# Optimization experiments

Measured on AMD Instinct MI355X. Metric: run time of the kernel, lower is better.

The kernel has to match this reference:

```python
import jax, jax.numpy as jnp
import numpy as np

N_NODES = 100000
N_EDGES = 1600000
F_IN, F1, F2, F3 = 128, 128, 128, 64


def setup_inputs() -> dict:
    key = jax.random.key(0)
    ks = jax.random.split(key, 10)
    edge_index = jax.random.randint(ks[0], (2, N_EDGES), 0, N_NODES, dtype=jnp.int64)
    x = jax.random.normal(ks[1], (N_NODES, F_IN), dtype=jnp.float32)
    def glorot(k, fi, fo):
        s = (6.0 / (fi + fo)) ** 0.5
        return jax.random.uniform(k, (fi, fo), jnp.float32, -s, s)
    return {
        "edge_index": edge_index,
        "x": x,
        "W1": glorot(ks[2], F_IN, F1), "b1": jnp.zeros((F1,), jnp.float32),
        "W2": glorot(ks[3], F1, F2), "b2": jnp.zeros((F2,), jnp.float32),
        "W3": glorot(ks[4], F2, F3), "b3": jnp.zeros((F3,), jnp.float32),
        "W_att": glorot(ks[5], F3, F3),
    }


def _gcn_conv(x, W, b, src, dst, deg_inv_sqrt):
    h = x @ W  # [N, Fo]
    norm = deg_inv_sqrt[src] * deg_inv_sqrt[dst]  # [E]
    agg = jax.ops.segment_sum(h[src] * norm[:, None], dst, num_segments=x.shape[0])
    agg = agg + h * (deg_inv_sqrt * deg_inv_sqrt)[:, None]  # self-loop term
    return agg + b


def _attention_pool(emb, W_att):
    # SimGNN attention pooling
    ctx = jnp.tanh(jnp.mean(emb @ W_att, axis=0))          # [F3]
    scores = jax.nn.sigmoid(emb @ ctx)                      # [N]
    return emb.T @ scores[:, None]                          # [F3, 1]


def reference(edge_index, x, W1, b1, W2, b2, W3, b3, W_att):
    src, dst = edge_index[0], edge_index[1]
    n = x.shape[0]
    deg = jax.ops.segment_sum(jnp.ones_like(src, dtype=x.dtype), dst, num_segments=n) + 1.0
    dis = jax.lax.rsqrt(deg)
    h = jax.nn.relu(_gcn_conv(x, W1, b1, src, dst, dis))
    h = jax.nn.relu(_gcn_conv(h, W2, b2, src, dst, dis))
    h = _gcn_conv(h, W3, b3, src, dst, dis)                 # abstract_features [N, F3]
    pooled = _attention_pool(h, W_att)                      # [F3, 1]
    return h, pooled
```

## Files before the change

kernel.cpp:

```cpp
#include <hip/hip_runtime.h>
#include <hip/hip_bf16.h>

#define NN 100000
#define NE 1600000
#define NR 100032
#define NB2 196
#define NBLK 391
#define EPB 4096

#if defined(__has_builtin)
#  if __has_builtin(__builtin_amdgcn_cvt_pk_f32_fp8) && \
      __has_builtin(__builtin_amdgcn_cvt_pk_fp8_f32) && \
      __has_builtin(__builtin_amdgcn_cvt_f32_fp8)
#    define HWF8 1
#  endif
#endif

typedef float f32x2 __attribute__((ext_vector_type(2)));
typedef float f32x4 __attribute__((ext_vector_type(4)));
typedef short bf16x8 __attribute__((ext_vector_type(8)));

static __device__ __forceinline__ float bf2f(__hip_bfloat16 v) { return __bfloat162float(v); }
static __device__ __forceinline__ float bfu(unsigned short w) {
    return __uint_as_float((unsigned)w << 16);
}

static __device__ __forceinline__ float f8d_sw(unsigned b) {
    unsigned e = (b >> 3) & 15u, m = b & 7u;
    float mag;
    if (e == 0) mag = (float)m * 0.001953125f;
    else        mag = __uint_as_float(((e + 120u) << 23) | (m << 20));
    return (b & 0x80u) ? -mag : mag;
}
static __device__ __forceinline__ unsigned char f8e_sw(float x) {
    unsigned u = __float_as_uint(x);
    unsigned s = (u >> 31) << 7;
    unsigned au = u & 0x7fffffffu;
    if (au >= 0x43E00000u) return (unsigned char)(s | 0x7Eu);
    if (au <  0x3A800000u) return (unsigned char)s;
    if (au <  0x3C800000u) {
        float a = __uint_as_float(au);
        int m = (int)rintf(a * 512.0f);
        if (m >= 8) return (unsigned char)(s | 0x08u);
        return (unsigned char)(s | (unsigned)m);
    }
    au += 0x80000u;
    if (au >= 0x43E00000u) return (unsigned char)(s | 0x7Eu);
    unsigned e = (au >> 23) - 120u;
    unsigned m = (au >> 20) & 7u;
    return (unsigned char)(s | (e << 3) | m);
}

static __device__ __forceinline__ float f8d1(unsigned b) {
#ifdef HWF8
    return __builtin_amdgcn_cvt_f32_fp8((int)b, 0);
#else
    return f8d_sw(b);
#endif
}
static __device__ __forceinline__ void f8d2(unsigned short v, float& x0, float& x1) {
#ifdef HWF8
    f32x2 r = __builtin_amdgcn_cvt_pk_f32_fp8((int)(unsigned)v, false);
    x0 = r.x; x1 = r.y;
#else
    x0 = f8d_sw(v & 255u); x1 = f8d_sw(v >> 8);
#endif
}
static __device__ __forceinline__ void f8d4(unsigned u, float* o) {
#ifdef HWF8
    f32x2 lo = __builtin_amdgcn_cvt_pk_f32_fp8((int)u, false);
    f32x2 hi = __builtin_amdgcn_cvt_pk_f32_fp8((int)u, true);
    o[0] = lo.x; o[1] = lo.y; o[2] = hi.x; o[3] = hi.y;
#else
    o[0] = f8d_sw(u & 255u); o[1] = f8d_sw((u >> 8) & 255u);
    o[2] = f8d_sw((u >> 16) & 255u); o[3] = f8d_sw(u >> 24);
#endif
}
static __device__ __forceinline__ unsigned short f8e2(float a, float b) {
#ifdef HWF8
    float ca = fminf(fmaxf(a, -448.0f), 448.0f);
    float cb = fminf(fmaxf(b, -448.0f), 448.0f);
    int p = __builtin_amdgcn_cvt_pk_fp8_f32(ca, cb, 0, false);
    return (unsigned short)(p & 0xFFFF);
#else
    return (unsigned short)f8e_sw(a) | ((unsigned short)f8e_sw(b) << 8);
#endif
}
static __device__ __forceinline__ unsigned char f8e1(float a) {
    return (unsigned char)(f8e2(a, 0.0f) & 0xFF);
}
static __device__ __forceinline__ unsigned bfpack(float lo, float hi) {
    return (__float_as_uint(lo) >> 16) | (__float_as_uint(hi) & 0xFFFF0000u);
}

static __device__ __forceinline__ void fma8(float* acc, uint2 v, float w) {
    float o[8];
    f8d4(v.x, o); f8d4(v.y, o + 4);
#pragma unroll
    for (int k = 0; k < 8; k++) acc[k] = fmaf(o[k], w, acc[k]);
}

__global__ void k_probe1(const unsigned short* __restrict__ xw,
                         const int* __restrict__ ei, int* __restrict__ raw) {
    int i = blockIdx.x * 256 + threadIdx.x;
    int nan = ((xw[i] & 0x7F80u) == 0x7F80u) ? 1 : 0;
    int odd = (ei[2 * i + 1] != 0) ? 1 : 0;
    unsigned long long bn = __ballot(nan);
    unsigned long long bo = __ballot(odd);
    if ((threadIdx.x & 63) == 0) {
        if (bn) atomicAdd(&raw[0], __popcll(bn));
        if (bo) atomicAdd(&raw[1], __popcll(bo));
    }
}
__global__ void k_probe2(const int* __restrict__ raw, int* __restrict__ flags) {
    if (threadIdx.x == 0) {
        flags[0] = (raw[0] > 0) ? 1 : 0;
        flags[1] = (raw[1] == 0) ? 1 : 0;
    }
}

static __device__ __forceinline__ int e_src(const int* ei, int e, int f64) {
    int v = f64 ? ei[2 * e] : ei[e];
    return min(max(v, 0), NN - 1);
}
static __device__ __forceinline__ int e_dst(const int* ei, int e, int f64) {
    int v = f64 ? ei[2 * (NE + e)] : ei[NE + e];
    return min(max(v, 0), NN - 1);
}
static __device__ __forceinline__ float ldx(const void* p, long long i, int f32) {
    return f32 ? ((const float*)p)[i] : bf2f(((const __hip_bfloat16*)p)[i]);
}

__global__ void cvt_params(const void* W1, const void* b1, const void* W2, const void* b2,
                           const void* W3, const void* b3, const void* Wa,
                           unsigned short* W1b, unsigned short* W2b, unsigned short* W3b,
                           float* b1f, float* b2f, float* b3f, float* Waf,
                           const int* flags) {
    int i = blockIdx.x * blockDim.x + threadIdx.x;
    int f = flags[0];
    if (i < 16384) {
        int j = i & 7, l = (i >> 3) & 63, c = (i >> 9) & 7, kc = i >> 12;
        int k = kc * 32 + ((l >> 4)) * 8 + j;
        int col = c * 16 + (l & 15);
        W1b[i] = __bfloat16_as_ushort(__float2bfloat16(ldx(W1, k * 128 + col, f)));
        W2b[i] = __bfloat16_as_ushort(__float2bfloat16(ldx(W2, k * 128 + col, f)));
    }
    if (i < 8192) {
        int j = i & 7, l = (i >> 3) & 63, c = (i >> 9) & 3, kc = i >> 11;
        int k = kc * 32 + ((l >> 4)) * 8 + j;
        int col = c * 16 + (l & 15);
        W3b[i] = __bfloat16_as_ushort(__float2bfloat16(ldx(W3, k * 64 + col, f)));
    }
    if (i < 4096)  Waf[i] = ldx(Wa, i, f);
    if (i < 128)   { b1f[i] = ldx(b1, i, f); b2f[i] = ldx(b2, i, f); }
    if (i < 64)    b3f[i] = ldx(b3, i, f);
}

__global__ void k_cvtx(const void* __restrict__ x, unsigned char* __restrict__ P,
                       const int* __restrict__ flags) {
    int i = blockIdx.x * blockDim.x + threadIdx.x;
    if (i >= (NN * 128) / 4) return;
    unsigned pk;
    if (flags[0]) {
        float4 v = ((const float4*)x)[i];
        pk = (unsigned)f8e2(v.x, v.y) | ((unsigned)f8e2(v.z, v.w) << 16);
    } else {
        ushort4 v = ((const ushort4*)x)[i];
        pk = (unsigned)f8e2(bfu(v.x), bfu(v.y)) | ((unsigned)f8e2(bfu(v.z), bfu(v.w)) << 16);
    }
    ((unsigned*)P)[i] = pk;
}

__global__ __launch_bounds__(256) void k_hist(const int* __restrict__ ei,
                                              int* __restrict__ ghist,
                                              const int* __restrict__ flags) {
    __shared__ int h[NB2];
    int blk = blockIdx.x, t = threadIdx.x;
    for (int i = t; i < NB2; i += 256) h[i] = 0;
    __syncthreads();
    int f64 = flags[1];
    int e0 = blk * EPB;
    for (int i = t; i < EPB; i += 256) {
        int e = e0 + i;
        if (e < NE) atomicAdd(&h[e_dst(ei, e, f64) >> 9], 1);
    }
    __syncthreads();
    for (int i = t; i < NB2; i += 256) ghist[blk * NB2 + i] = h[i];
}

__global__ __launch_bounds__(256) void k_off(const int* __restrict__ ghist,
                                             int* __restrict__ cbase,
                                             int* __restrict__ offm,
                                             int* __restrict__ rowptr) {
    __shared__ int tot[NB2];
    int t = threadIdx.x;
    if (t < NB2) {
        int s = 0;
        for (int blk = 0; blk < NBLK; blk++) s += ghist[blk * NB2 + t];
        tot[t] = s;
    }
    __syncthreads();
    if (t == 0) {
        int run = 0;
        for (int b = 0; b < NB2; b++) { cbase[b] = run; run += tot[b]; }
        cbase[NB2] = run;
        rowptr[NN] = run;
    }
    __syncthreads();
    if (t < NB2) {
        int run = cbase[t];
        for (int blk = 0; blk < NBLK; blk++) {
            offm[blk * NB2 + t] = run;
            run += ghist[blk * NB2 + t];
        }
    }
}

__global__ __launch_bounds__(256) void k_scatter(const int* __restrict__ ei,
                                                 const int* __restrict__ offm,
                                                 int* __restrict__ scratch,
                                                 const int* __restrict__ flags) {
    __shared__ int cur[NB2];
    int blk = blockIdx.x, t = threadIdx.x;
    for (int i = t; i < NB2; i += 256) cur[i] = offm[blk * NB2 + i];
    __syncthreads();
    int f64 = flags[1];
    int e0 = blk * EPB;
    for (int i = t; i < EPB; i += 256) {
        int e = e0 + i;
        if (e < NE) {
            int d = e_dst(ei, e, f64);
            int s = e_src(ei, e, f64);
            int p = atomicAdd(&cur[d >> 9], 1);
            p = min(max(p, 0), NE - 1);
            scratch[p] = s | ((d & 511) << 17);
        }
    }
}

__global__ __launch_bounds__(256) void k_build(const int* __restrict__ scratch,
                                               const int* __restrict__ cbase,
                                               int* __restrict__ rowptr,
                                               float* __restrict__ dis,
                                               int* __restrict__ csr) {
    __shared__ int hist[512];
    __shared__ int base[512];
    __shared__ int sd[256];
    int b = blockIdx.x, t = threadIdx.x;
    int n0 = b << 9;
    int s0 = cbase[b], s1 = cbase[b + 1];
    hist[t] = 0; hist[t + 256] = 0;
    __syncthreads();
    for (int i = s0 + t; i < s1; i += 256) {
        int dlo = (scratch[i] >> 17) & 511;
        atomicAdd(&hist[dlo], 1);
    }
    __syncthreads();
    int v0 = hist[2 * t], v1 = hist[2 * t + 1];
    int s = v0 + v1;
    sd[t] = s; __syncthreads();
    for (int o = 1; o < 256; o <<= 1) {
        int add = (t >= o) ? sd[t - o] : 0;
        __syncthreads();
        sd[t] += add;
        __syncthreads();
    }
    int run = s0 + sd[t] - s;
    base[2 * t] = run;
    base[2 * t + 1] = run + v0;
    int n = n0 + 2 * t;
    if (n < NN) {
        rowptr[n] = run;
        dis[n] = rsqrtf((float)v0 + 1.0f);
    }
    if (n + 1 < NN) {
        rowptr[n + 1] = run + v0;
        dis[n + 1] = rsqrtf((float)v1 + 1.0f);
    }
    __syncthreads();
    for (int i = s0 + t; i < s1; i += 256) {
        int v = scratch[i];
        int dlo = (v >> 17) & 511;
        int p = atomicAdd(&base[dlo], 1);
        p = min(max(p, 0), NE - 1);
        csr[p] = v & 0x1FFFF;
    }
}

template <int NCT>
__global__ __launch_bounds__(256) void k_xf_mfma(const unsigned char* __restrict__ A,
                                                 const unsigned short* __restrict__ Wf,
                                                 unsigned char* __restrict__ O) {
    __shared__ unsigned short wl[NCT * 4 * 64 * 8];
    int t = threadIdx.x;
    int n0 = blockIdx.x * 64;
    {
        const uint4* wg = (const uint4*)Wf;
        uint4* wld = (uint4*)wl;
#pragma unroll
        for (int i = 0; i < NCT; i++) wld[i * 256 + t] = wg[i * 256 + t];
    }
    __syncthreads();
    int w = t >> 6, l = t & 63;
    int quad = l >> 4, m = l & 15;
    int arow = n0 + w * 16 + m;
    const unsigned char* ap = A + (size_t)arow * 128 + quad * 8;
    f32x4 acc[NCT];
#pragma unroll
    for (int c = 0; c < NCT; c++) acc[c] = (f32x4){0.0f, 0.0f, 0.0f, 0.0f};
#pragma unroll
    for (int kc = 0; kc < 4; kc++) {
        uint2 g = *(const uint2*)(ap + kc * 32);
        float o[8];
        f8d4(g.x, o); f8d4(g.y, o + 4);
        union { unsigned u[4]; bf16x8 v; } fr;
        fr.u[0] = bfpack(o[0], o[1]);
        fr.u[1] = bfpack(o[2], o[3]);
        fr.u[2] = bfpack(o[4], o[5]);
        fr.u[3] = bfpack(o[6], o[7]);
#pragma unroll
        for (int c = 0; c < NCT; c++) {
            bf16x8 bw = *(const bf16x8*)&wl[((kc * NCT + c) * 64 + l) * 8];
            acc[c] = __builtin_amdgcn_mfma_f32_16x16x32_bf16(fr.v, bw, acc[c], 0, 0, 0);
        }
    }
    int orow0 = n0 + w * 16 + quad * 4;
#pragma unroll
    for (int c = 0; c < NCT; c++) {
        int col = c * 16 + m;
#pragma unroll
        for (int r = 0; r < 4; r++) {
            int row = orow0 + r;
            if (row < NN) O[(size_t)row * (NCT * 16) + col] = f8e1(acc[c][r]);
        }
    }
}

template <bool RELU>
__global__ __launch_bounds__(256) void k_agg128(const unsigned char* __restrict__ Tb,
                                                const int* __restrict__ rowptr,
                                                const int* __restrict__ csr,
                                                const float* __restrict__ dis,
                                                const float* __restrict__ bias,
                                                unsigned char* __restrict__ H) {
    int n = blockIdx.x * 4 + (threadIdx.x >> 6);
    int lane = threadIdx.x & 63;
    int r = lane >> 4;
    int f = lane & 15;
    int fo = f << 3;
    float dn = dis[n];
    int s0 = rowptr[n], s1 = rowptr[n + 1];
    s0 = min(max(s0, 0), NE); s1 = min(max(s1, s0), NE);
    float acc[8];
#pragma unroll
    for (int k = 0; k < 8; k++) acc[k] = 0.0f;
    {
        uint2 v = *(const uint2*)(Tb + (((unsigned)n << 7) + (unsigned)fo));
        fma8(acc, v, (r == 0) ? dn : 0.0f);
    }
    int pa = r << 2;
    for (int base = s0; base < s1; base += 64) {
        int m = min(64, s1 - base);
        unsigned voff = 0u, wbits = 0u;
        if (lane < m) {
            int ss = csr[base + lane];
            ss = min(max(ss, 0), NN - 1);
            voff  = (unsigned)ss << 7;
            wbits = __float_as_uint(dis[ss]);
        }
        int ng  = (m + 3) >> 2;
        int ngp = (ng + 1) & ~1;
        for (int g = 0; g < ngp; g += 2) {
            int a0 = pa + (g << 4);
            unsigned vo0 = (unsigned)__builtin_amdgcn_ds_bpermute(a0,      (int)voff);
            unsigned wb0 = (unsigned)__builtin_amdgcn_ds_bpermute(a0,      (int)wbits);
            unsigned vo1 = (unsigned)__builtin_amdgcn_ds_bpermute(a0 + 16, (int)voff);
            unsigned wb1 = (unsigned)__builtin_amdgcn_ds_bpermute(a0 + 16, (int)wbits);
            uint2 v0 = *(const uint2*)(Tb + (vo0 + (unsigned)fo));
            uint2 v1 = *(const uint2*)(Tb + (vo1 + (unsigned)fo));
            fma8(acc, v0, __uint_as_float(wb0));
            fma8(acc, v1, __uint_as_float(wb1));
        }
    }
#pragma unroll
    for (int k = 0; k < 8; k++) {
        acc[k] += __shfl_xor(acc[k], 16, 64);
        acc[k] += __shfl_xor(acc[k], 32, 64);
    }
    float4 bA = *(const float4*)(bias + fo);
    float4 bB = *(const float4*)(bias + fo + 4);
    float t[8];
    t[0] = acc[0] * dn + bA.x; t[1] = acc[1] * dn + bA.y;
    t[2] = acc[2] * dn + bA.z; t[3] = acc[3] * dn + bA.w;
    t[4] = acc[4] * dn + bB.x; t[5] = acc[5] * dn + bB.y;
    t[6] = acc[6] * dn + bB.z; t[7] = acc[7] * dn + bB.w;
    if (RELU) {
#pragma unroll
        for (int k = 0; k < 8; k++) t[k] = fmaxf(t[k], 0.0f);
    }
    if (r == 0) {
        unsigned lo = (unsigned)f8e2(t[0], t[1]) | ((unsigned)f8e2(t[2], t[3]) << 16);
        unsigned hi = (unsigned)f8e2(t[4], t[5]) | ((unsigned)f8e2(t[6], t[7]) << 16);
        *(uint2*)(H + (((size_t)n << 7) + (size_t)fo)) = make_uint2(lo, hi);
    }
}

__global__ __launch_bounds__(256) void k_agg64(const unsigned char* __restrict__ Tb,
                                               const int* __restrict__ rowptr,
                                               const int* __restrict__ csr,
                                               const float* __restrict__ dis,
                                               const float* __restrict__ bias,
                                               unsigned short* __restrict__ Hb) {
    int n = blockIdx.x * 4 + (threadIdx.x >> 6);
    int lane = threadIdx.x & 63;
    int r = lane >> 3;
    int f = lane & 7;
    int fo = f << 3;
    float dn = dis[n];
    int s0 = rowptr[n], s1 = rowptr[n + 1];
    s0 = min(max(s0, 0), NE); s1 = min(max(s1, s0), NE);
    float acc[8];
#pragma unroll
    for (int k = 0; k < 8; k++) acc[k] = 0.0f;
    {
        uint2 v = *(const uint2*)(Tb + (((unsigned)n << 6) + (unsigned)fo));
        fma8(acc, v, (r == 0) ? dn : 0.0f);
    }
    int pa = r << 2;
    for (int base = s0; base < s1; base += 64) {
        int m = min(64, s1 - base);
        unsigned voff = 0u, wbits = 0u;
        if (lane < m) {
            int ss = csr[base + lane];
            ss = min(max(ss, 0), NN - 1);
            voff  = (unsigned)ss << 6;
            wbits = __float_as_uint(dis[ss]);
        }
        int ng  = (m + 7) >> 3;
        int ngp = (ng + 1) & ~1;
        for (int g = 0; g < ngp; g += 2) {
            int a0 = pa + (g << 5);
            unsigned vo0 = (unsigned)__builtin_amdgcn_ds_bpermute(a0,      (int)voff);
            unsigned wb0 = (unsigned)__builtin_amdgcn_ds_bpermute(a0,      (int)wbits);
            unsigned vo1 = (unsigned)__builtin_amdgcn_ds_bpermute(a0 + 32, (int)voff);
            unsigned wb1 = (unsigned)__builtin_amdgcn_ds_bpermute(a0 + 32, (int)wbits);
            uint2 v0 = *(const uint2*)(Tb + (vo0 + (unsigned)fo));
            uint2 v1 = *(const uint2*)(Tb + (vo1 + (unsigned)fo));
            fma8(acc, v0, __uint_as_float(wb0));
            fma8(acc, v1, __uint_as_float(wb1));
        }
    }
#pragma unroll
    for (int k = 0; k < 8; k++) {
        acc[k] += __shfl_xor(acc[k], 8, 64);
        acc[k] += __shfl_xor(acc[k], 16, 64);
        acc[k] += __shfl_xor(acc[k], 32, 64);
    }
    float4 bA = *(const float4*)(bias + fo);
    float4 bB = *(const float4*)(bias + fo + 4);
    float t[8];
    t[0] = acc[0] * dn + bA.x; t[1] = acc[1] * dn + bA.y;
    t[2] = acc[2] * dn + bA.z; t[3] = acc[3] * dn + bA.w;
    t[4] = acc[4] * dn + bB.x; t[5] = acc[5] * dn + bB.y;
    t[6] = acc[6] * dn + bB.z; t[7] = acc[7] * dn + bB.w;
    if (r == 0) {
        unsigned p0 = (unsigned)__bfloat16_as_ushort(__float2bfloat16(t[0])) |
                      ((unsigned)__bfloat16_as_ushort(__float2bfloat16(t[1])) << 16);
        unsigned p1 = (unsigned)__bfloat16_as_ushort(__float2bfloat16(t[2])) |
                      ((unsigned)__bfloat16_as_ushort(__float2bfloat16(t[3])) << 16);
        unsigned p2 = (unsigned)__bfloat16_as_ushort(__float2bfloat16(t[4])) |
                      ((unsigned)__bfloat16_as_ushort(__float2bfloat16(t[5])) << 16);
        unsigned p3 = (unsigned)__bfloat16_as_ushort(__float2bfloat16(t[6])) |
                      ((unsigned)__bfloat16_as_ushort(__float2bfloat16(t[7])) << 16);
        *(uint4*)(Hb + (((size_t)n << 6) + (size_t)fo)) = make_uint4(p0, p1, p2, p3);
    }
}

__global__ __launch_bounds__(512) void k_colsum(const unsigned short* __restrict__ h3,
                                                float* __restrict__ colsum) {
    int t = threadIdx.x;
    int lane = t & 63;
    int rg = lane >> 4, cq = lane & 15;
    int wid = (blockIdx.x * 512 + t) >> 6;
    int nw = (gridDim.x * 512) >> 6;
    float a0 = 0, a1 = 0, a2 = 0, a3 = 0;
    for (int r = wid * 4 + rg; r < NN; r += nw * 4) {
        uint2 v = *(const uint2*)(h3 + ((size_t)r << 6) + cq * 4);
        a0 += bfu((unsigned short)(v.x & 0xFFFF));
        a1 += bfu((unsigned short)(v.x >> 16));
        a2 += bfu((unsigned short)(v.y & 0xFFFF));
        a3 += bfu((unsigned short)(v.y >> 16));
    }
    a0 += __shfl_xor(a0, 16, 64); a0 += __shfl_xor(a0, 32, 64);
    a1 += __shfl_xor(a1, 16, 64); a1 += __shfl_xor(a1, 32, 64);
    a2 += __shfl_xor(a2, 16, 64); a2 += __shfl_xor(a2, 32, 64);
    a3 += __shfl_xor(a3, 16, 64); a3 += __shfl_xor(a3, 32, 64);
    __shared__ float part[8][64];
    int w = t >> 6;
    if (rg == 0) {
        part[w][cq * 4 + 0] = a0;
        part[w][cq * 4 + 1] = a1;
        part[w][cq * 4 + 2] = a2;
        part[w][cq * 4 + 3] = a3;
    }
    __syncthreads();
    if (t < 64) {
        float s = 0;
#pragma unroll
        for (int i = 0; i < 8; i++) s += part[i][t];
        atomicAdd(&colsum[t], s);
    }
}

__global__ void k_ctx(const float* __restrict__ colsum, const float* __restrict__ Wa,
                      float* __restrict__ ctx) {
    __shared__ float ms[64];
    int j = threadIdx.x;
    ms[j] = colsum[j] * (1.0f / NN);
    __syncthreads();
    float s = 0.0f;
#pragma unroll
    for (int k = 0; k < 64; k++) s += ms[k] * Wa[k * 64 + j];
    ctx[j] = tanhf(s);
}

__global__ __launch_bounds__(512) void k_pool(const unsigned short* __restrict__ h3,
                                              const float* __restrict__ ctx,
                                              float* __restrict__ pooled) {
    int t = threadIdx.x;
    int lane = t & 63;
    int rg = lane >> 4, cq = lane & 15;
    int wid = (blockIdx.x * 512 + t) >> 6;
    int nw = (gridDim.x * 512) >> 6;
    float c0 = ctx[cq * 4 + 0], c1 = ctx[cq * 4 + 1];
    float c2 = ctx[cq * 4 + 2], c3 = ctx[cq * 4 + 3];
    float q0 = 0, q1 = 0, q2 = 0, q3 = 0;
    for (int r = wid * 4 + rg; r < NN; r += nw * 4) {
        uint2 v = *(const uint2*)(h3 + ((size_t)r << 6) + cq * 4);
        float x0 = bfu((unsigned short)(v.x & 0xFFFF));
        float x1 = bfu((unsigned short)(v.x >> 16));
        float x2 = bfu((unsigned short)(v.y & 0xFFFF));
        float x3 = bfu((unsigned short)(v.y >> 16));
        float p = x0 * c0 + x1 * c1 + x2 * c2 + x3 * c3;
        p += __shfl_xor(p, 1, 64);
        p += __shfl_xor(p, 2, 64);
        p += __shfl_xor(p, 4, 64);
        p += __shfl_xor(p, 8, 64);
        float sc = 1.0f / (1.0f + expf(-p));
        q0 += sc * x0; q1 += sc * x1; q2 += sc * x2; q3 += sc * x3;
    }
    q0 += __shfl_xor(q0, 16, 64); q0 += __shfl_xor(q0, 32, 64);
    q1 += __shfl_xor(q1, 16, 64); q1 += __shfl_xor(q1, 32, 64);
    q2 += __shfl_xor(q2, 16, 64); q2 += __shfl_xor(q2, 32, 64);
    q3 += __shfl_xor(q3, 16, 64); q3 += __shfl_xor(q3, 32, 64);
    __shared__ float part[8][64];
    int w = t >> 6;
    if (rg == 0) {
        part[w][cq * 4 + 0] = q0;
        part[w][cq * 4 + 1] = q1;
        part[w][cq * 4 + 2] = q2;
        part[w][cq * 4 + 3] = q3;
    }
    __syncthreads();
    if (t < 64) {
        float s = 0;
#pragma unroll
        for (int i = 0; i < 8; i++) s += part[i][t];
        atomicAdd(&pooled[t], s);
    }
}

__global__ void k_out(const unsigned short* __restrict__ h3, const float* __restrict__ pooled,
                      void* __restrict__ out, const int* __restrict__ flags) {
    int q = blockIdx.x * blockDim.x + threadIdx.x;
    if (q >= 1600016) return;
    long long i0 = (long long)q * 4;
    float v[4];
#pragma unroll
    for (int k = 0; k < 4; k++) {
        long long i = i0 + k;
        v[k] = (i < 6400000LL) ? bfu(h3[i]) : pooled[i - 6400000LL];
    }
    if (flags[0]) {
        *(float4*)((float*)out + i0) = make_float4(v[0], v[1], v[2], v[3]);
    } else {
        unsigned lo = (unsigned)__bfloat16_as_ushort(__float2bfloat16(v[0])) |
                      ((unsigned)__bfloat16_as_ushort(__float2bfloat16(v[1])) << 16);
        unsigned hi = (unsigned)__bfloat16_as_ushort(__float2bfloat16(v[2])) |
                      ((unsigned)__bfloat16_as_ushort(__float2bfloat16(v[3])) << 16);
        *(uint2*)((unsigned short*)out + i0) = make_uint2(lo, hi);
    }
}

static constexpr size_t AL(size_t x) { return (x + 255) & ~size_t(255); }
static constexpr size_t OFF_FLAGS  = 0;
static constexpr size_t OFF_RAW    = OFF_FLAGS + 256;
static constexpr size_t OFF_GHIST  = OFF_RAW + 256;
static constexpr size_t OFF_OFFM   = OFF_GHIST + AL((size_t)NBLK * NB2 * 4);
static constexpr size_t OFF_CBASE  = OFF_OFFM + AL((size_t)NBLK * NB2 * 4);
static constexpr size_t OFF_ROWPTR = OFF_CBASE + AL((NB2 + 1) * 4);
static constexpr size_t OFF_CSR    = OFF_ROWPTR + AL((NN + 1) * 4);
static constexpr size_t OFF_DIS    = OFF_CSR + AL((size_t)NE * 4);
static constexpr size_t OFF_P      = OFF_DIS + AL(NN * 4);
static constexpr size_t OFF_W1B    = OFF_P + AL((size_t)NR * 128);
static constexpr size_t OFF_W2B    = OFF_W1B + AL(16384 * 2);
static constexpr size_t OFF_W3B    = OFF_W2B + AL(16384 * 2);
static constexpr size_t OFF_B1F    = OFF_W3B + AL(8192 * 2);
static constexpr size_t OFF_B2F    = OFF_B1F + AL(128 * 4);
static constexpr size_t OFF_B3F    = OFF_B2F + AL(128 * 4);
static constexpr size_t OFF_WAF    = OFF_B3F + AL(64 * 4);
static constexpr size_t OFF_COLSUM = OFF_WAF + AL(4096 * 4);
static constexpr size_t OFF_POOLED = OFF_COLSUM + AL(64 * 4);
static constexpr size_t OFF_CTX    = OFF_POOLED + AL(64 * 4);

extern "C" void kernel_launch(void* const* d_in, const int* in_sizes, int n_in,
                              void* d_out, int out_size, void* d_ws, size_t ws_size,
                              hipStream_t stream) {
    const int* ei = (const int*)d_in[0];
    const void* x  = d_in[1];
    const void* W1 = d_in[2];
    const void* b1 = d_in[3];
    const void* W2 = d_in[4];
    const void* b2 = d_in[5];
    const void* W3 = d_in[6];
    const void* b3 = d_in[7];
    const void* Wa = d_in[8];

    char* ws = (char*)d_ws;
    int*   flags  = (int*)(ws + OFF_FLAGS);
    int*   raw    = (int*)(ws + OFF_RAW);
    int*   ghist  = (int*)(ws + OFF_GHIST);
    int*   offm   = (int*)(ws + OFF_OFFM);
    int*   cbase  = (int*)(ws + OFF_CBASE);
    int*   rowptr = (int*)(ws + OFF_ROWPTR);
    int*   csr    = (int*)(ws + OFF_CSR);
    float* dis    = (float*)(ws + OFF_DIS);
    unsigned char*  P    = (unsigned char*)(ws + OFF_P);
    int*            scrA = (int*)(ws + OFF_P);
    unsigned short* Hb   = (unsigned short*)(ws + OFF_P);
    unsigned short* W1b = (unsigned short*)(ws + OFF_W1B);
    unsigned short* W2b = (unsigned short*)(ws + OFF_W2B);
    unsigned short* W3b = (unsigned short*)(ws + OFF_W3B);
    float* b1f    = (float*)(ws + OFF_B1F);
    float* b2f    = (float*)(ws + OFF_B2F);
    float* b3f    = (float*)(ws + OFF_B3F);
    float* Waf    = (float*)(ws + OFF_WAF);
    float* colsum = (float*)(ws + OFF_COLSUM);
    float* pooled = (float*)(ws + OFF_POOLED);
    float* ctx    = (float*)(ws + OFF_CTX);

    unsigned char* Q = (unsigned char*)d_out;

    hipMemsetAsync(raw, 0, 256, stream);
    hipMemsetAsync(colsum, 0, 64 * 4, stream);
    hipMemsetAsync(pooled, 0, 64 * 4, stream);

    k_probe1<<<256, 256, 0, stream>>>((const unsigned short*)x, ei, raw);
    k_probe2<<<1, 64, 0, stream>>>(raw, flags);
    cvt_params<<<64, 256, 0, stream>>>(W1, b1, W2, b2, W3, b3, Wa,
                                       W1b, W2b, W3b, b1f, b2f, b3f, Waf, flags);

    k_hist<<<NBLK, 256, 0, stream>>>(ei, ghist, flags);
    k_off<<<1, 256, 0, stream>>>(ghist, cbase, offm, rowptr);
    k_scatter<<<NBLK, 256, 0, stream>>>(ei, offm, scrA, flags);
    k_build<<<NB2, 256, 0, stream>>>(scrA, cbase, rowptr, dis, csr);

    k_cvtx<<<(NN * 128 / 4 + 255) / 256, 256, 0, stream>>>(x, P, flags);

    k_xf_mfma<8><<<NR / 64, 256, 0, stream>>>(P, W1b, Q);
    k_agg128<true><<<NN / 4, 256, 0, stream>>>(Q, rowptr, csr, dis, b1f, P);
    k_xf_mfma<8><<<NR / 64, 256, 0, stream>>>(P, W2b, Q);
    k_agg128<true><<<NN / 4, 256, 0, stream>>>(Q, rowptr, csr, dis, b2f, P);
    k_xf_mfma<4><<<NR / 64, 256, 0, stream>>>(P, W3b, Q);
    k_agg64<<<NN / 4, 256, 0, stream>>>(Q, rowptr, csr, dis, b3f, Hb);

    k_colsum<<<256, 512, 0, stream>>>(Hb, colsum);
    k_ctx<<<1, 64, 0, stream>>>(colsum, Waf, ctx);
    k_pool<<<256, 512, 0, stream>>>(Hb, ctx, pooled);

    k_out<<<(1600016 + 255) / 256, 256, 0, stream>>>(Hb, pooled, d_out, flags);
}
```

Measured before the change: 422.8 us.

## Pre-scale transformed features by source degree norm and widen gather loads

The source-side normalization dis[src] is folded into the feature transform output, so the aggregation kernels no longer load or shuffle per-edge weights and can simply add gathered rows. Each lane now gathers 16 fp8 features (uint4) instead of 8, halving lanes per row, and accumulation uses packed fp8-to-f32x2 conversions. A zero pad row at index NN is written and used as the dummy gather target. The aim is to cut per-edge memory and permute traffic, in exchange for a longer reduction tree and a pre-scaled fp8 quantization that may shift numerics.

```diff
diff --git a/kernel.cpp b/kernel.cpp
--- a/kernel.cpp
+++ b/kernel.cpp
@@ -93,11 +93,46 @@
     return (__float_as_uint(lo) >> 16) | (__float_as_uint(hi) & 0xFFFF0000u);
 }
 
-static __device__ __forceinline__ void fma8(float* acc, uint2 v, float w) {
-    float o[8];
-    f8d4(v.x, o); f8d4(v.y, o + 4);
-#pragma unroll
-    for (int k = 0; k < 8; k++) acc[k] = fmaf(o[k], w, acc[k]);
+static __device__ __forceinline__ void acc16_add(f32x2* acc, uint4 v) {
+#ifdef HWF8
+    acc[0] += __builtin_amdgcn_cvt_pk_f32_fp8((int)v.x, false);
+    acc[1] += __builtin_amdgcn_cvt_pk_f32_fp8((int)v.x, true);
+    acc[2] += __builtin_amdgcn_cvt_pk_f32_fp8((int)v.y, false);
+    acc[3] += __builtin_amdgcn_cvt_pk_f32_fp8((int)v.y, true);
+    acc[4] += __builtin_amdgcn_cvt_pk_f32_fp8((int)v.z, false);
+    acc[5] += __builtin_amdgcn_cvt_pk_f32_fp8((int)v.z, true);
+    acc[6] += __builtin_amdgcn_cvt_pk_f32_fp8((int)v.w, false);
+    acc[7] += __builtin_amdgcn_cvt_pk_f32_fp8((int)v.w, true);
+#else
+    unsigned u[4] = {v.x, v.y, v.z, v.w};
+#pragma unroll
+    for (int q = 0; q < 4; q++) {
+        float o[4]; f8d4(u[q], o);
+        acc[2 * q]     += (f32x2){o[0], o[1]};
+        acc[2 * q + 1] += (f32x2){o[2], o[3]};
+    }
+#endif
+}
+static __device__ __forceinline__ void acc16_fma(f32x2* acc, uint4 v, float w) {
+    f32x2 wv = (f32x2){w, w};
+#ifdef HWF8
+    acc[0] += __builtin_amdgcn_cvt_pk_f32_fp8((int)v.x, false) * wv;
+    acc[1] += __builtin_amdgcn_cvt_pk_f32_fp8((int)v.x, true)  * wv;
+    acc[2] += __builtin_amdgcn_cvt_pk_f32_fp8((int)v.y, false) * wv;
+    acc[3] += __builtin_amdgcn_cvt_pk_f32_fp8((int)v.y, true)  * wv;
+    acc[4] += __builtin_amdgcn_cvt_pk_f32_fp8((int)v.z, false) * wv;
+    acc[5] += __builtin_amdgcn_cvt_pk_f32_fp8((int)v.z, true)  * wv;
+    acc[6] += __builtin_amdgcn_cvt_pk_f32_fp8((int)v.w, false) * wv;
+    acc[7] += __builtin_amdgcn_cvt_pk_f32_fp8((int)v.w, true)  * wv;
+#else
+    unsigned u[4] = {v.x, v.y, v.z, v.w};
+#pragma unroll
+    for (int q = 0; q < 4; q++) {
+        float o[4]; f8d4(u[q], o);
+        acc[2 * q]     += (f32x2){o[0] * w, o[1] * w};
+        acc[2 * q + 1] += (f32x2){o[2] * w, o[3] * w};
+    }
+#endif
 }
 
 __global__ void k_probe1(const unsigned short* __restrict__ xw,
@@ -290,6 +325,7 @@
 template <int NCT>
 __global__ __launch_bounds__(256) void k_xf_mfma(const unsigned char* __restrict__ A,
                                                  const unsigned short* __restrict__ Wf,
+                                                 const float* __restrict__ dis,
                                                  unsigned char* __restrict__ O) {
     __shared__ unsigned short wl[NCT * 4 * 64 * 8];
     int t = threadIdx.x;
@@ -325,13 +361,19 @@
         }
     }
     int orow0 = n0 + w * 16 + quad * 4;
+    float dsc[4];
+#pragma unroll
+    for (int r = 0; r < 4; r++) {
+        int row = orow0 + r;
+        dsc[r] = (row < NN) ? dis[row] : 0.0f;
+    }
 #pragma unroll
     for (int c = 0; c < NCT; c++) {
         int col = c * 16 + m;
 #pragma unroll
         for (int r = 0; r < 4; r++) {
             int row = orow0 + r;
-            if (row < NN) O[(size_t)row * (NCT * 16) + col] = f8e1(acc[c][r]);
+            if (row <= NN) O[(size_t)row * (NCT * 16) + col] = f8e1(acc[c][r] * dsc[r]);
         }
     }
 }
@@ -345,63 +387,72 @@
                                                 unsigned char* __restrict__ H) {
     int n = blockIdx.x * 4 + (threadIdx.x >> 6);
     int lane = threadIdx.x & 63;
-    int r = lane >> 4;
-    int f = lane & 15;
-    int fo = f << 3;
+    int r = lane >> 3;
+    int f = lane & 7;
+    int fo = f << 4;
     float dn = dis[n];
     int s0 = rowptr[n], s1 = rowptr[n + 1];
     s0 = min(max(s0, 0), NE); s1 = min(max(s1, s0), NE);
-    float acc[8];
-#pragma unroll
-    for (int k = 0; k < 8; k++) acc[k] = 0.0f;
+    f32x2 acc[8];
+#pragma unroll
+    for (int k = 0; k < 8; k++) acc[k] = (f32x2){0.0f, 0.0f};
     {
-        uint2 v = *(const uint2*)(Tb + (((unsigned)n << 7) + (unsigned)fo));
-        fma8(acc, v, (r == 0) ? dn : 0.0f);
+        uint4 v = *(const uint4*)(Tb + (((unsigned)n << 7) + (unsigned)fo));
+        acc16_fma(acc, v, (r == 0) ? 1.0f : 0.0f);
     }
     int pa = r << 2;
     for (int base = s0; base < s1; base += 64) {
         int m = min(64, s1 - base);
-        unsigned voff = 0u, wbits = 0u;
+        unsigned voff = (unsigned)NN << 7;
         if (lane < m) {
             int ss = csr[base + lane];
             ss = min(max(ss, 0), NN - 1);
-            voff  = (unsigned)ss << 7;
-            wbits = __float_as_uint(dis[ss]);
-        }
-        int ng  = (m + 3) >> 2;
+            voff = (unsigned)ss << 7;
+        }
+        int ng  = (m + 7) >> 3;
         int ngp = (ng + 1) & ~1;
         for (int g = 0; g < ngp; g += 2) {
-            int a0 = pa + (g << 4);
+            int a0 = pa + (g << 5);
             unsigned vo0 = (unsigned)__builtin_amdgcn_ds_bpermute(a0,      (int)voff);
-            unsigned wb0 = (unsigned)__builtin_amdgcn_ds_bpermute(a0,      (int)wbits);
-            unsigned vo1 = (unsigned)__builtin_amdgcn_ds_bpermute(a0 + 16, (int)voff);
-            unsigned wb1 = (unsigned)__builtin_amdgcn_ds_bpermute(a0 + 16, (int)wbits);
-            uint2 v0 = *(const uint2*)(Tb + (vo0 + (unsigned)fo));
-            uint2 v1 = *(const uint2*)(Tb + (vo1 + (unsigned)fo));
-            fma8(acc, v0, __uint_as_float(wb0));
-            fma8(acc, v1, __uint_as_float(wb1));
+            unsigned vo1 = (unsigned)__builtin_amdgcn_ds_bpermute(a0 + 32, (int)voff);
+            uint4 v0 = *(const uint4*)(Tb + (vo0 + (unsigned)fo));
+            uint4 v1 = *(const uint4*)(Tb + (vo1 + (unsigned)fo));
+            acc16_add(acc, v0);
+            acc16_add(acc, v1);
         }
     }
 #pragma unroll
     for (int k = 0; k < 8; k++) {
-        acc[k] += __shfl_xor(acc[k], 16, 64);
-        acc[k] += __shfl_xor(acc[k], 32, 64);
-    }
-    float4 bA = *(const float4*)(bias + fo);
-    float4 bB = *(const float4*)(bias + fo + 4);
-    float t[8];
-    t[0] = acc[0] * dn + bA.x; t[1] = acc[1] * dn + bA.y;
-    t[2] = acc[2] * dn + bA.z; t[3] = acc[3] * dn + bA.w;
-    t[4] = acc[4] * dn + bB.x; t[5] = acc[5] * dn + bB.y;
-    t[6] = acc[6] * dn + bB.z; t[7] = acc[7] * dn + bB.w;
-    if (RELU) {
-#pragma unroll
-        for (int k = 0; k < 8; k++) t[k] = fmaxf(t[k], 0.0f);
+        acc[k].x += __shfl_xor(acc[k].x, 8, 64);
+        acc[k].y += __shfl_xor(acc[k].y, 8, 64);
+        acc[k].x += __shfl_xor(acc[k].x, 16, 64);
+        acc[k].y += __shfl_xor(acc[k].y, 16, 64);
+        acc[k].x += __shfl_xor(acc[k].x, 32, 64);
+        acc[k].y += __shfl_xor(acc[k].y, 32, 64);
     }
     if (r == 0) {
-        unsigned lo = (unsigned)f8e2(t[0], t[1]) | ((unsigned)f8e2(t[2], t[3]) << 16);
-        unsigned hi = (unsigned)f8e2(t[4], t[5]) | ((unsigned)f8e2(t[6], t[7]) << 16);
-        *(uint2*)(H + (((size_t)n << 7) + (size_t)fo)) = make_uint2(lo, hi);
+        float4 B0 = *(const float4*)(bias + 16 * f);
+        float4 B1 = *(const float4*)(bias + 16 * f + 4);
+        float4 B2 = *(const float4*)(bias + 16 * f + 8);
+        float4 B3 = *(const float4*)(bias + 16 * f + 12);
+        float bb[16] = {B0.x, B0.y, B0.z, B0.w, B1.x, B1.y, B1.z, B1.w,
+                        B2.x, B2.y, B2.z, B2.w, B3.x, B3.y, B3.z, B3.w};
+        float t[16];
+#pragma unroll
+        for (int k = 0; k < 8; k++) {
+            t[2 * k]     = acc[k].x * dn + bb[2 * k];
+            t[2 * k + 1] = acc[k].y * dn + bb[2 * k + 1];
+        }
+        if (RELU) {
+#pragma unroll
+            for (int k = 0; k < 16; k++) t[k] = fmaxf(t[k], 0.0f);
+        }
+        uint4 o;
+        o.x = (unsigned)f8e2(t[0],  t[1])  | ((unsigned)f8e2(t[2],  t[3])  << 16);
+        o.y = (unsigned)f8e2(t[4],  t[5])  | ((unsigned)f8e2(t[6],  t[7])  << 16);
+        o.z = (unsigned)f8e2(t[8],  t[9])  | ((unsigned)f8e2(t[10], t[11]) << 16);
+        o.w = (unsigned)f8e2(t[12], t[13]) | ((unsigned)f8e2(t[14], t[15]) << 16);
+        *(uint4*)(H + (((size_t)n << 7) + (size_t)fo)) = o;
     }
 }
 
@@ -413,66 +464,72 @@
                                                unsigned short* __restrict__ Hb) {
     int n = blockIdx.x * 4 + (threadIdx.x >> 6);
     int lane = threadIdx.x & 63;
-    int r = lane >> 3;
-    int f = lane & 7;
-    int fo = f << 3;
+    int r = lane >> 2;
+    int f = lane & 3;
+    int fo = f << 4;
     float dn = dis[n];
     int s0 = rowptr[n], s1 = rowptr[n + 1];
     s0 = min(max(s0, 0), NE); s1 = min(max(s1, s0), NE);
-    float acc[8];
-#pragma unroll
-    for (int k = 0; k < 8; k++) acc[k] = 0.0f;
+    f32x2 acc[8];
+#pragma unroll
+    for (int k = 0; k < 8; k++) acc[k] = (f32x2){0.0f, 0.0f};
     {
-        uint2 v = *(const uint2*)(Tb + (((unsigned)n << 6) + (unsigned)fo));
-        fma8(acc, v, (r == 0) ? dn : 0.0f);
+        uint4 v = *(const uint4*)(Tb + (((unsigned)n << 6) + (unsigned)fo));
+        acc16_fma(acc, v, (r == 0) ? 1.0f : 0.0f);
     }
     int pa = r << 2;
     for (int base = s0; base < s1; base += 64) {
         int m = min(64, s1 - base);
-        unsigned voff = 0u, wbits = 0u;
+        unsigned voff = (unsigned)NN << 6;
         if (lane < m) {
             int ss = csr[base + lane];
             ss = min(max(ss, 0), NN - 1);
-            voff  = (unsigned)ss << 6;
-            wbits = __float_as_uint(dis[ss]);
-        }
-        int ng  = (m + 7) >> 3;
+            voff = (unsigned)ss << 6;
+        }
+        int ng  = (m + 15) >> 4;
         int ngp = (ng + 1) & ~1;
         for (int g = 0; g < ngp; g += 2) {
-            int a0 = pa + (g << 5);
+            int a0 = pa + (g << 6);
             unsigned vo0 = (unsigned)__builtin_amdgcn_ds_bpermute(a0,      (int)voff);
-            unsigned wb0 = (unsigned)__builtin_amdgcn_ds_bpermute(a0,      (int)wbits);
-            unsigned vo1 = (unsigned)__builtin_amdgcn_ds_bpermute(a0 + 32, (int)voff);
-            unsigned wb1 = (unsigned)__builtin_amdgcn_ds_bpermute(a0 + 32, (int)wbits);
-            uint2 v0 = *(const uint2*)(Tb + (vo0 + (unsigned)fo));
-            uint2 v1 = *(const uint2*)(Tb + (vo1 + (unsigned)fo));
-            fma8(acc, v0, __uint_as_float(wb0));
-            fma8(acc, v1, __uint_as_float(wb1));
+            unsigned vo1 = (unsigned)__builtin_amdgcn_ds_bpermute(a0 + 64, (int)voff);
+            uint4 v0 = *(const uint4*)(Tb + (vo0 + (unsigned)fo));
+            uint4 v1 = *(const uint4*)(Tb + (vo1 + (unsigned)fo));
+            acc16_add(acc, v0);
+            acc16_add(acc, v1);
         }
     }
 #pragma unroll
     for (int k = 0; k < 8; k++) {
-        acc[k] += __shfl_xor(acc[k], 8, 64);
-        acc[k] += __shfl_xor(acc[k], 16, 64);
-        acc[k] += __shfl_xor(acc[k], 32, 64);
-    }
-    float4 bA = *(const float4*)(bias + fo);
-    float4 bB = *(const float4*)(bias + fo + 4);
-    float t[8];
-    t[0] = acc[0] * dn + bA.x; t[1] = acc[1] * dn + bA.y;
-    t[2] = acc[2] * dn + bA.z; t[3] = acc[3] * dn + bA.w;
-    t[4] = acc[4] * dn + bB.x; t[5] = acc[5] * dn + bB.y;
-    t[6] = acc[6] * dn + bB.z; t[7] = acc[7] * dn + bB.w;
+        acc[k].x += __shfl_xor(acc[k].x, 4, 64);
+        acc[k].y += __shfl_xor(acc[k].y, 4, 64);
+        acc[k].x += __shfl_xor(acc[k].x, 8, 64);
+        acc[k].y += __shfl_xor(acc[k].y, 8, 64);
+        acc[k].x += __shfl_xor(acc[k].x, 16, 64);
+        acc[k].y += __shfl_xor(acc[k].y, 16, 64);
+        acc[k].x += __shfl_xor(acc[k].x, 32, 64);
+        acc[k].y += __shfl_xor(acc[k].y, 32, 64);
+    }
     if (r == 0) {
-        unsigned p0 = (unsigned)__bfloat16_as_ushort(__float2bfloat16(t[0])) |
-                      ((unsigned)__bfloat16_as_ushort(__float2bfloat16(t[1])) << 16);
-        unsigned p1 = (unsigned)__bfloat16_as_ushort(__float2bfloat16(t[2])) |
-                      ((unsigned)__bfloat16_as_ushort(__float2bfloat16(t[3])) << 16);
-        unsigned p2 = (unsigned)__bfloat16_as_ushort(__float2bfloat16(t[4])) |
-                      ((unsigned)__bfloat16_as_ushort(__float2bfloat16(t[5])) << 16);
-        unsigned p3 = (unsigned)__bfloat16_as_ushort(__float2bfloat16(t[6])) |
-                      ((unsigned)__bfloat16_as_ushort(__float2bfloat16(t[7])) << 16);
-        *(uint4*)(Hb + (((size_t)n << 6) + (size_t)fo)) = make_uint4(p0, p1, p2, p3);
+        float4 B0 = *(const float4*)(bias + 16 * f);
+        float4 B1 = *(const float4*)(bias + 16 * f + 4);
+        float4 B2 = *(const float4*)(bias + 16 * f + 8);
+        float4 B3 = *(const float4*)(bias + 16 * f + 12);
+        float bb[16] = {B0.x, B0.y, B0.z, B0.w, B1.x, B1.y, B1.z, B1.w,
+                        B2.x, B2.y, B2.z, B2.w, B3.x, B3.y, B3.z, B3.w};
+        float t[16];
+#pragma unroll
+        for (int k = 0; k < 8; k++) {
+            t[2 * k]     = acc[k].x * dn + bb[2 * k];
+            t[2 * k + 1] = acc[k].y * dn + bb[2 * k + 1];
+        }
+        unsigned p[8];
+#pragma unroll
+        for (int k = 0; k < 8; k++)
+            p[k] = (unsigned)__bfloat16_as_ushort(__float2bfloat16(t[2 * k])) |
+                   ((unsigned)__bfloat16_as_ushort(__float2bfloat16(t[2 * k + 1])) << 16);
+        unsigned short* op = Hb + (((size_t)n << 6) + (size_t)(f * 16));
+        *(uint4*)op       = make_uint4(p[0], p[1], p[2], p[3]);
+        *(uint4*)(op + 8) = make_uint4(p[4], p[5], p[6], p[7]);
     }
 }
 
@@ -667,11 +724,11 @@
 
     k_cvtx<<<(NN * 128 / 4 + 255) / 256, 256, 0, stream>>>(x, P, flags);
 
-    k_xf_mfma<8><<<NR / 64, 256, 0, stream>>>(P, W1b, Q);
+    k_xf_mfma<8><<<NR / 64, 256, 0, stream>>>(P, W1b, dis, Q);
     k_agg128<true><<<NN / 4, 256, 0, stream>>>(Q, rowptr, csr, dis, b1f, P);
-    k_xf_mfma<8><<<NR / 64, 256, 0, stream>>>(P, W2b, Q);
+    k_xf_mfma<8><<<NR / 64, 256, 0, stream>>>(P, W2b, dis, Q);
     k_agg128<true><<<NN / 4, 256, 0, stream>>>(Q, rowptr, csr, dis, b2f, P);
-    k_xf_mfma<4><<<NR / 64, 256, 0, stream>>>(P, W3b, Q);
+    k_xf_mfma<4><<<NR / 64, 256, 0, stream>>>(P, W3b, dis, Q);
     k_agg64<<<NN / 4, 256, 0, stream>>>(Q, rowptr, csr, dis, b3f, Hb);
 
     k_colsum<<<256, 512, 0, stream>>>(Hb, colsum);
```

After: 487.5 us. 1.15x slower.

## Fold source-degree scaling into transform output and pack 64-wide aggregation

Applied to the files above, without the earlier changes.

The transform kernel now multiplies each output row by its inverse-sqrt degree before fp8 quantization, so aggregation becomes a plain sum and no longer needs per-edge dis gathers or the weight bpermutes. Accumulation uses packed f32x2 adds with hardware fp8 pair conversion. The 64-feature aggregation now handles two nodes per wavefront with 32-lane halves. A zero padding row at index NN is written and used for inactive lanes. Pre-scaling changes fp8 quantization ranges, and correctness depends on padding row NN being zero, which requires dis[NN] to be read as 0.

```diff
diff --git a/kernel.cpp b/kernel.cpp
--- a/kernel.cpp
+++ b/kernel.cpp
@@ -93,11 +93,38 @@
     return (__float_as_uint(lo) >> 16) | (__float_as_uint(hi) & 0xFFFF0000u);
 }
 
-static __device__ __forceinline__ void fma8(float* acc, uint2 v, float w) {
-    float o[8];
-    f8d4(v.x, o); f8d4(v.y, o + 4);
-#pragma unroll
-    for (int k = 0; k < 8; k++) acc[k] = fmaf(o[k], w, acc[k]);
+static __device__ __forceinline__ void acc8_add(f32x2* acc, uint2 v) {
+#ifdef HWF8
+    acc[0] += __builtin_amdgcn_cvt_pk_f32_fp8((int)v.x, false);
+    acc[1] += __builtin_amdgcn_cvt_pk_f32_fp8((int)v.x, true);
+    acc[2] += __builtin_amdgcn_cvt_pk_f32_fp8((int)v.y, false);
+    acc[3] += __builtin_amdgcn_cvt_pk_f32_fp8((int)v.y, true);
+#else
+    unsigned u[2] = {v.x, v.y};
+#pragma unroll
+    for (int q = 0; q < 2; q++) {
+        float o[4]; f8d4(u[q], o);
+        acc[2 * q]     += (f32x2){o[0], o[1]};
+        acc[2 * q + 1] += (f32x2){o[2], o[3]};
+    }
+#endif
+}
+static __device__ __forceinline__ void acc8_fma(f32x2* acc, uint2 v, float w) {
+    f32x2 wv = (f32x2){w, w};
+#ifdef HWF8
+    acc[0] += __builtin_amdgcn_cvt_pk_f32_fp8((int)v.x, false) * wv;
+    acc[1] += __builtin_amdgcn_cvt_pk_f32_fp8((int)v.x, true)  * wv;
+    acc[2] += __builtin_amdgcn_cvt_pk_f32_fp8((int)v.y, false) * wv;
+    acc[3] += __builtin_amdgcn_cvt_pk_f32_fp8((int)v.y, true)  * wv;
+#else
+    unsigned u[2] = {v.x, v.y};
+#pragma unroll
+    for (int q = 0; q < 2; q++) {
+        float o[4]; f8d4(u[q], o);
+        acc[2 * q]     += (f32x2){o[0] * w, o[1] * w};
+        acc[2 * q + 1] += (f32x2){o[2] * w, o[3] * w};
+    }
+#endif
 }
 
 __global__ void k_probe1(const unsigned short* __restrict__ xw,
@@ -290,6 +317,7 @@
 template <int NCT>
 __global__ __launch_bounds__(256) void k_xf_mfma(const unsigned char* __restrict__ A,
                                                  const unsigned short* __restrict__ Wf,
+                                                 const float* __restrict__ dis,
                                                  unsigned char* __restrict__ O) {
     __shared__ unsigned short wl[NCT * 4 * 64 * 8];
     int t = threadIdx.x;
@@ -325,13 +353,19 @@
         }
     }
     int orow0 = n0 + w * 16 + quad * 4;
+    float dsc[4];
+#pragma unroll
+    for (int r = 0; r < 4; r++) {
+        int row = orow0 + r;
+        dsc[r] = (row < NN) ? dis[row] : 0.0f;
+    }
 #pragma unroll
     for (int c = 0; c < NCT; c++) {
         int col = c * 16 + m;
 #pragma unroll
         for (int r = 0; r < 4; r++) {
             int row = orow0 + r;
-            if (row < NN) O[(size_t)row * (NCT * 16) + col] = f8e1(acc[c][r]);
+            if (row <= NN) O[(size_t)row * (NCT * 16) + col] = f8e1(acc[c][r] * dsc[r]);
         }
     }
 }
@@ -351,54 +385,58 @@
     float dn = dis[n];
     int s0 = rowptr[n], s1 = rowptr[n + 1];
     s0 = min(max(s0, 0), NE); s1 = min(max(s1, s0), NE);
-    float acc[8];
-#pragma unroll
-    for (int k = 0; k < 8; k++) acc[k] = 0.0f;
+    f32x2 acc[4];
+#pragma unroll
+    for (int k = 0; k < 4; k++) acc[k] = (f32x2){0.0f, 0.0f};
     {
         uint2 v = *(const uint2*)(Tb + (((unsigned)n << 7) + (unsigned)fo));
-        fma8(acc, v, (r == 0) ? dn : 0.0f);
-    }
-    int pa = r << 2;
+        acc8_fma(acc, v, (r == 0) ? 1.0f : 0.0f);
+    }
     for (int base = s0; base < s1; base += 64) {
         int m = min(64, s1 - base);
-        unsigned voff = 0u, wbits = 0u;
+        unsigned voff = (unsigned)NN << 7;
         if (lane < m) {
             int ss = csr[base + lane];
             ss = min(max(ss, 0), NN - 1);
-            voff  = (unsigned)ss << 7;
-            wbits = __float_as_uint(dis[ss]);
-        }
-        int ng  = (m + 3) >> 2;
-        int ngp = (ng + 1) & ~1;
-        for (int g = 0; g < ngp; g += 2) {
-            int a0 = pa + (g << 4);
+            voff = (unsigned)ss << 7;
+        }
+        int ng = (m + 3) >> 2;
+        int g = 0;
+        for (; g + 2 <= ng; g += 2) {
+            int a0 = (g * 4 + r) * 4;
             unsigned vo0 = (unsigned)__builtin_amdgcn_ds_bpermute(a0,      (int)voff);
-            unsigned wb0 = (unsigned)__builtin_amdgcn_ds_bpermute(a0,      (int)wbits);
             unsigned vo1 = (unsigned)__builtin_amdgcn_ds_bpermute(a0 + 16, (int)voff);
-            unsigned wb1 = (unsigned)__builtin_amdgcn_ds_bpermute(a0 + 16, (int)wbits);
             uint2 v0 = *(const uint2*)(Tb + (vo0 + (unsigned)fo));
             uint2 v1 = *(const uint2*)(Tb + (vo1 + (unsigned)fo));
-            fma8(acc, v0, __uint_as_float(wb0));
-            fma8(acc, v1, __uint_as_float(wb1));
-        }
-    }
-#pragma unroll
-    for (int k = 0; k < 8; k++) {
-        acc[k] += __shfl_xor(acc[k], 16, 64);
-        acc[k] += __shfl_xor(acc[k], 32, 64);
-    }
-    float4 bA = *(const float4*)(bias + fo);
-    float4 bB = *(const float4*)(bias + fo + 4);
-    float t[8];
-    t[0] = acc[0] * dn + bA.x; t[1] = acc[1] * dn + bA.y;
-    t[2] = acc[2] * dn + bA.z; t[3] = acc[3] * dn + bA.w;
-    t[4] = acc[4] * dn + bB.x; t[5] = acc[5] * dn + bB.y;
-    t[6] = acc[6] * dn + bB.z; t[7] = acc[7] * dn + bB.w;
-    if (RELU) {
-#pragma unroll
-        for (int k = 0; k < 8; k++) t[k] = fmaxf(t[k], 0.0f);
+            acc8_add(acc, v0);
+            acc8_add(acc, v1);
+        }
+        if (g < ng) {
+            int a0 = (g * 4 + r) * 4;
+            unsigned vo0 = (unsigned)__builtin_amdgcn_ds_bpermute(a0, (int)voff);
+            uint2 v0 = *(const uint2*)(Tb + (vo0 + (unsigned)fo));
+            acc8_add(acc, v0);
+        }
+    }
+#pragma unroll
+    for (int k = 0; k < 4; k++) {
+        acc[k].x += __shfl_xor(acc[k].x, 16, 64);
+        acc[k].y += __shfl_xor(acc[k].y, 16, 64);
+        acc[k].x += __shfl_xor(acc[k].x, 32, 64);
+        acc[k].y += __shfl_xor(acc[k].y, 32, 64);
     }
     if (r == 0) {
+        float4 bA = *(const float4*)(bias + fo);
+        float4 bB = *(const float4*)(bias + fo + 4);
+        float t[8];
+        t[0] = acc[0].x * dn + bA.x; t[1] = acc[0].y * dn + bA.y;
+        t[2] = acc[1].x * dn + bA.z; t[3] = acc[1].y * dn + bA.w;
+        t[4] = acc[2].x * dn + bB.x; t[5] = acc[2].y * dn + bB.y;
+        t[6] = acc[3].x * dn + bB.z; t[7] = acc[3].y * dn + bB.w;
+        if (RELU) {
+#pragma unroll
+            for (int k = 0; k < 8; k++) t[k] = fmaxf(t[k], 0.0f);
+        }
         unsigned lo = (unsigned)f8e2(t[0], t[1]) | ((unsigned)f8e2(t[2], t[3]) << 16);
         unsigned hi = (unsigned)f8e2(t[4], t[5]) | ((unsigned)f8e2(t[6], t[7]) << 16);
         *(uint2*)(H + (((size_t)n << 7) + (size_t)fo)) = make_uint2(lo, hi);
@@ -411,59 +449,65 @@
                                                const float* __restrict__ dis,
                                                const float* __restrict__ bias,
                                                unsigned short* __restrict__ Hb) {
-    int n = blockIdx.x * 4 + (threadIdx.x >> 6);
     int lane = threadIdx.x & 63;
-    int r = lane >> 3;
-    int f = lane & 7;
+    int half = lane >> 5;
+    int hl = lane & 31;
+    int n = blockIdx.x * 8 + (threadIdx.x >> 6) * 2 + half;
+    int r = hl >> 3;
+    int f = hl & 7;
     int fo = f << 3;
     float dn = dis[n];
     int s0 = rowptr[n], s1 = rowptr[n + 1];
     s0 = min(max(s0, 0), NE); s1 = min(max(s1, s0), NE);
-    float acc[8];
-#pragma unroll
-    for (int k = 0; k < 8; k++) acc[k] = 0.0f;
+    f32x2 acc[4];
+#pragma unroll
+    for (int k = 0; k < 4; k++) acc[k] = (f32x2){0.0f, 0.0f};
     {
         uint2 v = *(const uint2*)(Tb + (((unsigned)n << 6) + (unsigned)fo));
-        fma8(acc, v, (r == 0) ? dn : 0.0f);
-    }
-    int pa = r << 2;
-    for (int base = s0; base < s1; base += 64) {
-        int m = min(64, s1 - base);
-        unsigned voff = 0u, wbits = 0u;
-        if (lane < m) {
-            int ss = csr[base + lane];
+        acc8_fma(acc, v, (r == 0) ? 1.0f : 0.0f);
+    }
+    int ab = half << 7;
+    for (int base = s0; base < s1; base += 32) {
+        int m = min(32, s1 - base);
+        unsigned voff = (unsigned)NN << 6;
+        if (hl < m) {
+            int ss = csr[base + hl];
             ss = min(max(ss, 0), NN - 1);
-            voff  = (unsigned)ss << 6;
-            wbits = __float_as_uint(dis[ss]);
-        }
-        int ng  = (m + 7) >> 3;
-        int ngp = (ng + 1) & ~1;
-        for (int g = 0; g < ngp; g += 2) {
-            int a0 = pa + (g << 5);
+            voff = (unsigned)ss << 6;
+        }
+        int ng = (m + 3) >> 2;
+        int g = 0;
+        for (; g + 2 <= ng; g += 2) {
+            int a0 = ab + (g * 4 + r) * 4;
             unsigned vo0 = (unsigned)__builtin_amdgcn_ds_bpermute(a0,      (int)voff);
-            unsigned wb0 = (unsigned)__builtin_amdgcn_ds_bpermute(a0,      (int)wbits);
-            unsigned vo1 = (unsigned)__builtin_amdgcn_ds_bpermute(a0 + 32, (int)voff);
-            unsigned wb1 = (unsigned)__builtin_amdgcn_ds_bpermute(a0 + 32, (int)wbits);
+            unsigned vo1 = (unsigned)__builtin_amdgcn_ds_bpermute(a0 + 16, (int)voff);
             uint2 v0 = *(const uint2*)(Tb + (vo0 + (unsigned)fo));
             uint2 v1 = *(const uint2*)(Tb + (vo1 + (unsigned)fo));
-            fma8(acc, v0, __uint_as_float(wb0));
-            fma8(acc, v1, __uint_as_float(wb1));
-        }
-    }
-#pragma unroll
-    for (int k = 0; k < 8; k++) {
-        acc[k] += __shfl_xor(acc[k], 8, 64);
-        acc[k] += __shfl_xor(acc[k], 16, 64);
-        acc[k] += __shfl_xor(acc[k], 32, 64);
-    }
-    float4 bA = *(const float4*)(bias + fo);
-    float4 bB = *(const float4*)(bias + fo + 4);
-    float t[8];
-    t[0] = acc[0] * dn + bA.x; t[1] = acc[1] * dn + bA.y;
-    t[2] = acc[2] * dn + bA.z; t[3] = acc[3] * dn + bA.w;
-    t[4] = acc[4] * dn + bB.x; t[5] = acc[5] * dn + bB.y;
-    t[6] = acc[6] * dn + bB.z; t[7] = acc[7] * dn + bB.w;
+            acc8_add(acc, v0);
+            acc8_add(acc, v1);
+        }
+        if (g < ng) {
+            int a0 = ab + (g * 4 + r) * 4;
+            unsigned vo0 = (unsigned)__builtin_amdgcn_ds_bpermute(a0, (int)voff);
+            uint2 v0 = *(const uint2*)(Tb + (vo0 + (unsigned)fo));
+            acc8_add(acc, v0);
+        }
+    }
+#pragma unroll
+    for (int k = 0; k < 4; k++) {
+        acc[k].x += __shfl_xor(acc[k].x, 8, 64);
+        acc[k].y += __shfl_xor(acc[k].y, 8, 64);
+        acc[k].x += __shfl_xor(acc[k].x, 16, 64);
+        acc[k].y += __shfl_xor(acc[k].y, 16, 64);
+    }
     if (r == 0) {
+        float4 bA = *(const float4*)(bias + fo);
+        float4 bB = *(const float4*)(bias + fo + 4);
+        float t[8];
+        t[0] = acc[0].x * dn + bA.x; t[1] = acc[0].y * dn + bA.y;
+        t[2] = acc[1].x * dn + bA.z; t[3] = acc[1].y * dn + bA.w;
+        t[4] = acc[2].x * dn + bB.x; t[5] = acc[2].y * dn + bB.y;
+        t[6] = acc[3].x * dn + bB.z; t[7] = acc[3].y * dn + bB.w;
         unsigned p0 = (unsigned)__bfloat16_as_ushort(__float2bfloat16(t[0])) |
                       ((unsigned)__bfloat16_as_ushort(__float2bfloat16(t[1])) << 16);
         unsigned p1 = (unsigned)__bfloat16_as_ushort(__float2bfloat16(t[2])) |
@@ -667,12 +711,12 @@
 
     k_cvtx<<<(NN * 128 / 4 + 255) / 256, 256, 0, stream>>>(x, P, flags);
 
-    k_xf_mfma<8><<<NR / 64, 256, 0, stream>>>(P, W1b, Q);
+    k_xf_mfma<8><<<NR / 64, 256, 0, stream>>>(P, W1b, dis, Q);
     k_agg128<true><<<NN / 4, 256, 0, stream>>>(Q, rowptr, csr, dis, b1f, P);
-    k_xf_mfma<8><<<NR / 64, 256, 0, stream>>>(P, W2b, Q);
+    k_xf_mfma<8><<<NR / 64, 256, 0, stream>>>(P, W2b, dis, Q);
     k_agg128<true><<<NN / 4, 256, 0, stream>>>(Q, rowptr, csr, dis, b2f, P);
-    k_xf_mfma<4><<<NR / 64, 256, 0, stream>>>(P, W3b, Q);
-    k_agg64<<<NN / 4, 256, 0, stream>>>(Q, rowptr, csr, dis, b3f, Hb);
+    k_xf_mfma<4><<<NR / 64, 256, 0, stream>>>(P, W3b, dis, Q);
+    k_agg64<<<NN / 8, 256, 0, stream>>>(Q, rowptr, csr, dis, b3f, Hb);
 
     k_colsum<<<256, 512, 0, stream>>>(Hb, colsum);
     k_ctx<<<1, 64, 0, stream>>>(colsum, Waf, ctx);
```

After: 416.2 us. No clear change (-1.6%).
